# Kernel optimization log

Measured on AMD Instinct MI355X. Metric: run time of the kernel, lower is better.

The kernel has to match this reference:

```python
import jax, jax.numpy as jnp
import numpy as np

B, L, D, H, R, E = 4, 2048, 256, 4, 128, 32768
HD = D // H  # head dim of long-range attention
FF = 4 * D   # positionwise FFN hidden
NEG_SLOPE = 0.2  # GATConv leaky_relu slope


def setup_inputs() -> dict:
    key = jax.random.key(0)
    ks = jax.random.split(key, 16)
    n = lambda k, sh: jax.random.normal(k, sh, dtype=jnp.float32) * 0.05
    z = lambda sh: jnp.zeros(sh, dtype=jnp.float32)
    o = lambda sh: jnp.ones(sh, dtype=jnp.float32)
    return {
        "s": jax.random.normal(ks[0], (B, L, D), dtype=jnp.float32),
        "gat_W": n(ks[1], (D, H * D)),
        "gat_att_src": n(ks[2], (H, D)),
        "gat_att_dst": n(ks[3], (H, D)),
        "gat_b": z((H * D,)),
        "short_W": n(ks[4], (H * D, D)), "short_b": z((D,)),
        "q_W": n(ks[5], (D, D)), "q_b": z((D,)),
        "k_W": n(ks[6], (D, D)), "k_b": z((D,)),
        "v_W": n(ks[7], (D, D)), "v_b": z((D,)),
        "o_W": n(ks[8], (D, D)), "o_b": z((D,)),
        "p_W": n(ks[9], (D, R)), "p_b": z((R,)),
        "lnq_g": o((D,)), "lnq_b": z((D,)),
        "lnk_g": o((D,)), "lnk_b": z((D,)),
        "lnv_g": o((D,)), "lnv_b": z((D,)),
        "ln1_g": o((D,)), "ln1_b": z((D,)),
        "ln2_g": o((D,)), "ln2_b": z((D,)),
        "f1_W": n(ks[10], (D, FF)), "f1_b": z((FF,)),
        "f2_W": n(ks[11], (FF, D)), "f2_b": z((D,)),
        "edge_index": jax.random.randint(ks[12], (2, E), 0, L, dtype=jnp.int32),
    }


def _ln(x, g, b, eps=1e-5):
    mu = jnp.mean(x, -1, keepdims=True)
    var = jnp.mean(jnp.square(x - mu), -1, keepdims=True)
    return (x - mu) * jax.lax.rsqrt(var + eps) * g + b


def _forward(p, edge_index):
    s = p["s"]
    loop = jnp.arange(L, dtype=edge_index.dtype)  # add_self_loops=True
    src = jnp.concatenate([edge_index[0], loop])
    dst = jnp.concatenate([edge_index[1], loop])

    def gat_one(x):  # x: [L, D] -> [L, H*D]  (PyG GATConv, concat=True)
        h = (x @ p["gat_W"]).reshape(L, H, D)
        a_src = jnp.einsum("nhc,hc->nh", h, p["gat_att_src"])
        a_dst = jnp.einsum("nhc,hc->nh", h, p["gat_att_dst"])
        e = jax.nn.leaky_relu(a_src[src] + a_dst[dst], NEG_SLOPE)  # [Etot, H]
        m = jax.ops.segment_max(e, dst, num_segments=L)            # scatter softmax
        ex = jnp.exp(e - m[dst])
        den = jax.ops.segment_sum(ex, dst, num_segments=L)
        alpha = ex / den[dst]
        out = jax.ops.segment_sum(h[src] * alpha[:, :, None], dst, num_segments=L)
        return out.reshape(L, H * D) + p["gat_b"]

    short = jax.vmap(gat_one)(s) @ p["short_W"] + p["short_b"]  # [B,L,D]

    # DynamicLongRange (Linformer-style dynamic projection)
    q = _ln(s @ p["q_W"] + p["q_b"], p["lnq_g"], p["lnq_b"])
    k = _ln(s @ p["k_W"] + p["k_b"], p["lnk_g"], p["lnk_b"])
    v = _ln(s @ p["v_W"] + p["v_b"], p["lnv_g"], p["lnv_b"])
    pm = jax.nn.softmax(k @ p["p_W"] + p["p_b"], axis=1)          # [B,L,R], softmax over seq
    k_c = jnp.einsum("blr,bld->brd", pm, k).reshape(B, R, H, HD)
    v_c = jnp.einsum("blr,bld->brd", pm, v).reshape(B, R, H, HD)
    q_h = q.reshape(B, L, H, HD)
    scores = jnp.einsum("blhd,brhd->bhlr", q_h, k_c) / jnp.sqrt(jnp.float32(HD))
    probs = jax.nn.softmax(scores, axis=-1)
    lng = jnp.einsum("bhlr,brhd->blhd", probs, v_c).reshape(B, L, D)
    lng = lng @ p["o_W"] + p["o_b"]

    # fuse short + long, residual + LN, then positionwise FFN + residual + LN
    h1 = _ln(s + short + lng, p["ln1_g"], p["ln1_b"])
    ff = jax.nn.relu(h1 @ p["f1_W"] + p["f1_b"]) @ p["f2_W"] + p["f2_b"]
    return _ln(h1 + ff, p["ln2_g"], p["ln2_b"])


def reference(s, gat_W, gat_att_src, gat_att_dst, gat_b, short_W, short_b,
              q_W, q_b, k_W, k_b, v_W, v_b, o_W, o_b, p_W, p_b,
              lnq_g, lnq_b, lnk_g, lnk_b, lnv_g, lnv_b,
              ln1_g, ln1_b, ln2_g, ln2_b, f1_W, f1_b, f2_W, f2_b, edge_index):
    p = dict(s=s, gat_W=gat_W, gat_att_src=gat_att_src, gat_att_dst=gat_att_dst,
             gat_b=gat_b, short_W=short_W, short_b=short_b, q_W=q_W, q_b=q_b,
             k_W=k_W, k_b=k_b, v_W=v_W, v_b=v_b, o_W=o_W, o_b=o_b, p_W=p_W,
             p_b=p_b, lnq_g=lnq_g, lnq_b=lnq_b, lnk_g=lnk_g, lnk_b=lnk_b,
             lnv_g=lnv_g, lnv_b=lnv_b, ln1_g=ln1_g, ln1_b=ln1_b, ln2_g=ln2_g,
             ln2_b=ln2_b, f1_W=f1_W, f1_b=f1_b, f2_W=f2_W, f2_b=f2_b)
    return _forward(p, edge_index)
```

## Files before the change

kernel.cpp:

```cpp
#include <hip/hip_runtime.h>
#include <math.h>

#define BB   4
#define LSEQ 2048
#define DV   256
#define HH   4
#define RR   128
#define EE   32768
#define ETOT (EE + LSEQ)
#define FFD  1024

typedef unsigned short u16;
typedef __attribute__((ext_vector_type(8))) short bf16x8;
typedef __attribute__((ext_vector_type(4))) float f32x4;

__device__ __forceinline__ u16 f2bf(float f) {
    union { float f; unsigned u; } x; x.f = f;
    unsigned r = x.u + 0x7fff + ((x.u >> 16) & 1);
    return (u16)(r >> 16);
}
__device__ __forceinline__ float bf2f(u16 u) {
    union { unsigned u; float f; } x; x.u = ((unsigned)u) << 16;
    return x.f;
}

__device__ __forceinline__ void gload16(const void* g, void* l) {
    __builtin_amdgcn_global_load_lds(
        (const __attribute__((address_space(1))) unsigned int*)g,
        (__attribute__((address_space(3))) unsigned int*)l, 16, 0, 0);
}

template<int BM, int BN, int OUTBF16, int ACT>
__global__ __launch_bounds__(256) void mfma_gemm_k(
    const u16* __restrict__ A, const u16* __restrict__ BT,
    const float* __restrict__ bias, void* __restrict__ Cv,
    int M, int N, int K, int lda, int ldb, int ldc,
    long bsA1, long bsA2, long bsB1, long bsB2, long bsC1, long bsC2,
    int subH, long pairB, long pairC, int ksl, int split, float alpha)
{
    constexpr int BK = 64;
    __shared__ u16 As[BM * BK];
    __shared__ u16 Bs[BN * BK];

    int z = blockIdx.z;
    int zb = z / subH, zh = z - zb * subH;
    int mtiles = M / BM;
    int pair = blockIdx.y / mtiles;
    int mt   = blockIdx.y - pair * mtiles;

    const u16* Ab = A  + zb * bsA1 + zh * bsA2;
    const u16* Bb = BT + zb * bsB1 + zh * bsB2 + (long)pair * pairB;
    int kstart = split ? zh * ksl : 0;
    int kcount = split ? ksl : K;
    int m0 = mt * BM, n0 = blockIdx.x * BN;

    int tid  = threadIdx.x;
    int wave = tid >> 6, lane = tid & 63;
    constexpr int WGN = (BN == 128) ? 2 : 1;
    constexpr int WGM = 4 / WGN;
    constexpr int MI  = BM / (WGM * 16);
    constexpr int NI  = BN / (WGN * 16);
    int wm = wave / WGN, wn = wave - wm * WGN;
    int wmo = wm * (MI * 16);
    int wno = wn * (NI * 16);

    f32x4 acc[MI][NI];
#pragma unroll
    for (int mi = 0; mi < MI; ++mi)
#pragma unroll
        for (int ni = 0; ni < NI; ++ni)
            acc[mi][ni] = (f32x4){0.f, 0.f, 0.f, 0.f};

    constexpr int AIT = (BM * BK / 8) / 256;
    constexpr int BIT = (BN * BK / 8) / 256;

    for (int k0 = 0; k0 < kcount; k0 += BK) {
        int kb = kstart + k0;
#pragma unroll
        for (int i = 0; i < AIT; ++i) {
            int p   = i * 256 + tid;
            int row = p >> 3;
            int kc  = (p & 7) ^ (row & 7);
            const u16* gp = Ab + (long)(m0 + row) * lda + kb + kc * 8;
            gload16(gp, (char*)As + (size_t)(i * 256 + wave * 64) * 16);
        }
#pragma unroll
        for (int i = 0; i < BIT; ++i) {
            int p   = i * 256 + tid;
            int row = p >> 3;
            int kc  = (p & 7) ^ (row & 7);
            const u16* gp = Bb + (long)(n0 + row) * ldb + kb + kc * 8;
            gload16(gp, (char*)Bs + (size_t)(i * 256 + wave * 64) * 16);
        }
        asm volatile("s_waitcnt vmcnt(0)");
        __syncthreads();

        const char* Ac = (const char*)As;
        const char* Bc = (const char*)Bs;
#pragma unroll
        for (int kh = 0; kh < 2; ++kh) {
            bf16x8 af[MI], bfr[NI];
            int kby = kh * 64 + ((lane >> 4) << 4);
#pragma unroll
            for (int mi = 0; mi < MI; ++mi) {
                int r = wmo + mi * 16 + (lane & 15);
                af[mi] = *(const bf16x8*)(Ac + r * 128 + (kby ^ ((r & 7) << 4)));
            }
#pragma unroll
            for (int ni = 0; ni < NI; ++ni) {
                int r = wno + ni * 16 + (lane & 15);
                bfr[ni] = *(const bf16x8*)(Bc + r * 128 + (kby ^ ((r & 7) << 4)));
            }
#pragma unroll
            for (int mi = 0; mi < MI; ++mi)
#pragma unroll
                for (int ni = 0; ni < NI; ++ni)
                    acc[mi][ni] = __builtin_amdgcn_mfma_f32_16x16x32_bf16(
                        af[mi], bfr[ni], acc[mi][ni], 0, 0, 0);
        }
        __syncthreads();
    }

    long cb = zb * bsC1 + zh * bsC2 + (long)pair * pairC;
#pragma unroll
    for (int mi = 0; mi < MI; ++mi) {
#pragma unroll
        for (int ni = 0; ni < NI; ++ni) {
            int col = n0 + wno + ni * 16 + (lane & 15);
            float bv = bias ? bias[col] : 0.f;
#pragma unroll
            for (int j = 0; j < 4; ++j) {
                int row = m0 + wmo + mi * 16 + ((lane >> 4) << 2) + j;
                float v = acc[mi][ni][j] * alpha + bv;
                if (ACT) v = fmaxf(v, 0.f);
                long idx = (long)row * ldc + col + cb;
                if (OUTBF16) ((u16*)Cv)[idx] = f2bf(v);
                else         ((float*)Cv)[idx] = v;
            }
        }
    }
}

__global__ __launch_bounds__(256) void attn_k(
    const u16* __restrict__ qb, const u16* __restrict__ kcb,
    const u16* __restrict__ vcT, u16* __restrict__ lngb)
{
    __shared__ u16 Ps[64 * 128];

    int bh = blockIdx.y;
    int b = bh >> 2, h = bh & 3;
    int l0 = blockIdx.x * 64;
    int tid = threadIdx.x, wave = tid >> 6, lane = tid & 63;
    int c = lane & 15, g = lane >> 4;

    const u16* kc = kcb + (long)b * (RR * DV) + h * 64;
    const u16* qg = qb + ((long)(b * LSEQ + l0)) * DV + h * 64;
    const u16* vg = vcT + ((long)b * DV + h * 64) * RR;

    f32x4 acc[8];
#pragma unroll
    for (int mi = 0; mi < 8; ++mi) acc[mi] = (f32x4){0.f, 0.f, 0.f, 0.f};

#pragma unroll
    for (int kh = 0; kh < 2; ++kh) {
        bf16x8 bq = *(const bf16x8*)(qg + (long)(wave * 16 + c) * DV + kh * 32 + g * 8);
#pragma unroll
        for (int mi = 0; mi < 8; ++mi) {
            bf16x8 af = *(const bf16x8*)(kc + (long)(mi * 16 + c) * DV + kh * 32 + g * 8);
            acc[mi] = __builtin_amdgcn_mfma_f32_16x16x32_bf16(af, bq, acc[mi], 0, 0, 0);
        }
    }

    float mx = -INFINITY;
#pragma unroll
    for (int mi = 0; mi < 8; ++mi)
#pragma unroll
        for (int j = 0; j < 4; ++j) {
            acc[mi][j] *= 0.125f;
            mx = fmaxf(mx, acc[mi][j]);
        }
    mx = fmaxf(mx, __shfl_xor(mx, 16));
    mx = fmaxf(mx, __shfl_xor(mx, 32));
    float den = 0.f;
#pragma unroll
    for (int mi = 0; mi < 8; ++mi)
#pragma unroll
        for (int j = 0; j < 4; ++j) {
            acc[mi][j] = __expf(acc[mi][j] - mx);
            den += acc[mi][j];
        }
    den += __shfl_xor(den, 16);
    den += __shfl_xor(den, 32);
    float inv = 1.0f / den;

    int l = wave * 16 + c;
#pragma unroll
    for (int mi = 0; mi < 8; ++mi) {
        short4 sv;
        sv.x = (short)f2bf(acc[mi][0] * inv);
        sv.y = (short)f2bf(acc[mi][1] * inv);
        sv.z = (short)f2bf(acc[mi][2] * inv);
        sv.w = (short)f2bf(acc[mi][3] * inv);
        int byte = l * 256 + ((mi * 32 + g * 8) ^ ((l & 7) << 4));
        *(short4*)((char*)Ps + byte) = sv;
    }
    __syncthreads();

    f32x4 a2[4];
#pragma unroll
    for (int ni = 0; ni < 4; ++ni) a2[ni] = (f32x4){0.f, 0.f, 0.f, 0.f};
#pragma unroll
    for (int kb = 0; kb < 4; ++kb) {
        int kby = kb * 64 + (g << 4);
        bf16x8 pa = *(const bf16x8*)((char*)Ps + l * 256 + (kby ^ ((l & 7) << 4)));
#pragma unroll
        for (int ni = 0; ni < 4; ++ni) {
            bf16x8 vf = *(const bf16x8*)(vg + (long)(ni * 16 + c) * RR + kb * 32 + g * 8);
            a2[ni] = __builtin_amdgcn_mfma_f32_16x16x32_bf16(pa, vf, a2[ni], 0, 0, 0);
        }
    }
#pragma unroll
    for (int ni = 0; ni < 4; ++ni)
#pragma unroll
        for (int j = 0; j < 4; ++j) {
            int lr = wave * 16 + g * 4 + j;
            int dh = ni * 16 + c;
            lngb[((long)(b * LSEQ + l0 + lr)) * DV + h * 64 + dh] = f2bf(a2[ni][j]);
        }
}

struct WTD { const float* src; u16* dst; int K, N, toff; };
struct WTA { WTD d[9]; };

__global__ __launch_bounds__(256) void wtrans_all_k(WTA a)
{
    int bid = blockIdx.x;
    int di = 0;
#pragma unroll
    for (int i = 1; i < 9; ++i) if (bid >= a.d[i].toff) di = i;
    const float* src = a.d[di].src;
    u16* dst = a.d[di].dst;
    int K = a.d[di].K, N = a.d[di].N;
    int tix = bid - a.d[di].toff;
    int nx = N >> 5;
    int tn = tix % nx, tk = tix / nx;
    int n0 = tn * 32, k0 = tk * 32;

    __shared__ float t[32][33];
    int tx = threadIdx.x & 31, ty = threadIdx.x >> 5;
#pragma unroll
    for (int i = 0; i < 32; i += 8)
        t[ty + i][tx] = src[(long)(k0 + ty + i) * N + n0 + tx];
    __syncthreads();
#pragma unroll
    for (int i = 0; i < 32; i += 8)
        dst[(long)(n0 + ty + i) * K + k0 + tx] = f2bf(t[tx][ty + i]);
}

__global__ __launch_bounds__(256) void ttrans_k(const u16* __restrict__ in,
                                                u16* __restrict__ out,
                                                int R, int C, long isb, long osb)
{
    in  += blockIdx.z * isb;
    out += blockIdx.z * osb;
    __shared__ u16 t[32][33];
    int c0 = blockIdx.x * 32, r0 = blockIdx.y * 32;
    int tx = threadIdx.x & 31, ty = threadIdx.x >> 5;
#pragma unroll
    for (int i = 0; i < 32; i += 8)
        t[ty + i][tx] = in[(long)(r0 + ty + i) * C + c0 + tx];
    __syncthreads();
#pragma unroll
    for (int i = 0; i < 32; i += 8)
        out[(long)(c0 + ty + i) * R + r0 + tx] = t[tx][ty + i];
}

__global__ void castcat_k(const float* __restrict__ in, u16* __restrict__ out,
                          const float* qb_, const float* kb_, const float* vb_,
                          float* qkvb, int* icnt)
{
    int bid = blockIdx.x;
    if (bid < 2048) {
        int i = (bid * 256 + threadIdx.x) * 4;
        float4 v = *(const float4*)(in + i);
        out[i]     = f2bf(v.x);
        out[i + 1] = f2bf(v.y);
        out[i + 2] = f2bf(v.z);
        out[i + 3] = f2bf(v.w);
    } else if (bid == 2048) {
        int i = threadIdx.x;
#pragma unroll
        for (int rep = 0; rep < 3; ++rep) {
            int j = i + rep * 256;
            qkvb[j] = (j < 256) ? qb_[j] : ((j < 512) ? kb_[j - 256] : vb_[j - 512]);
        }
    } else {
        int t = (bid - 2049) * 256 + threadIdx.x;
        if (t < 512) ((int4*)icnt)[t] = (int4){0, 0, 0, 0};
    }
}

__global__ __launch_bounds__(256) void gat_att_k(
    const u16* __restrict__ h, const float* __restrict__ att_src,
    const float* __restrict__ att_dst, float* __restrict__ a_src,
    float* __restrict__ a_dst)
{
    int row  = blockIdx.x * 4 + (threadIdx.x >> 6);
    int lane = threadIdx.x & 63;
    int c0   = lane * 16;
    int head = lane >> 4;

    float as[16], ad[16];
#pragma unroll
    for (int i = 0; i < 16; ++i) { as[i] = att_src[c0 + i]; ad[i] = att_dst[c0 + i]; }

    const u16* hr = h + (long)row * (HH * DV) + c0;
    bf16x8 v0 = *(const bf16x8*)(hr);
    bf16x8 v1 = *(const bf16x8*)(hr + 8);
    float ps = 0.f, pd = 0.f;
#pragma unroll
    for (int i = 0; i < 8; ++i) {
        float f0 = bf2f((u16)v0[i]), f1 = bf2f((u16)v1[i]);
        ps += f0 * as[i] + f1 * as[i + 8];
        pd += f0 * ad[i] + f1 * ad[i + 8];
    }
#pragma unroll
    for (int m = 1; m <= 8; m <<= 1) {
        ps += __shfl_xor(ps, m);
        pd += __shfl_xor(pd, m);
    }
    if ((lane & 15) == 0) {
        a_src[(long)row * HH + head] = ps;
        a_dst[(long)row * HH + head] = pd;
    }
}

__global__ void csr_count_k(const int* __restrict__ ei, int* __restrict__ cnt)
{
    int i = blockIdx.x * blockDim.x + threadIdx.x;
    if (i >= ETOT) return;
    int dst = (i < EE) ? ei[EE + i] : (i - EE);
    atomicAdd(&cnt[dst], 1);
}

__global__ __launch_bounds__(256) void csr_scan_k(const int* __restrict__ cnt, int* __restrict__ off)
{
    __shared__ int chunk[256];
    int tid = threadIdx.x;
    int base = tid * 8;
    int loc[8];
    int s = 0;
#pragma unroll
    for (int i = 0; i < 8; ++i) { loc[i] = s; s += cnt[base + i]; }
    chunk[tid] = s;
    __syncthreads();
    for (int st = 1; st < 256; st <<= 1) {
        int v = (tid >= st) ? chunk[tid - st] : 0;
        __syncthreads();
        chunk[tid] += v;
        __syncthreads();
    }
    int pre = (tid == 0) ? 0 : chunk[tid - 1];
#pragma unroll
    for (int i = 0; i < 8; ++i) off[base + i] = pre + loc[i];
    if (tid == 255) off[LSEQ] = chunk[255];
}

__global__ void csr_fill_k(const int* __restrict__ ei, const int* __restrict__ off,
                           int* __restrict__ cnt, int* __restrict__ bucket)
{
    int i = blockIdx.x * blockDim.x + threadIdx.x;
    if (i >= ETOT) return;
    int dst = (i < EE) ? ei[EE + i] : (i - EE);
    int p = atomicSub(&cnt[dst], 1) - 1;
    bucket[off[dst] + p] = i;
}

__global__ __launch_bounds__(256) void gat_gather_k(
    const u16* __restrict__ h, const int* __restrict__ ei,
    const int* __restrict__ off, const int* __restrict__ bucket,
    const float* __restrict__ a_src, const float* __restrict__ a_dst,
    const float* __restrict__ gat_b, u16* __restrict__ out)
{
    int wv = threadIdx.x >> 6, lane = threadIdx.x & 63;
    int n = blockIdx.x * 4 + wv;
    int b = blockIdx.y;
    int beg = off[n], deg = off[n + 1] - beg;

    __shared__ int   src_sh[4][64];
    __shared__ float ex_sh[4][64][4];

    const float* asrc_b = a_src + (long)b * LSEQ * HH;
    const float4 ad4 = *(const float4*)(a_dst + ((long)b * LSEQ + n) * HH);
    float adst[4] = { ad4.x, ad4.y, ad4.z, ad4.w };

    int hd = lane >> 4;
    const u16* hb = h + (long)b * LSEQ * (HH * DV) + lane * 16;
    float acc[16];
#pragma unroll
    for (int i = 0; i < 16; ++i) acc[i] = 0.f;
    float sm[4] = { 0.f, 0.f, 0.f, 0.f };

    for (int c0 = 0; c0 < deg; c0 += 64) {
        int idx = c0 + lane;
        if (idx < deg) {
            int eid = bucket[beg + idx];
            int src = (eid < EE) ? ei[eid] : (eid - EE);
            src_sh[wv][lane] = src;
            float4 as4 = *(const float4*)(asrc_b + (long)src * HH);
            float as[4] = { as4.x, as4.y, as4.z, as4.w };
#pragma unroll
            for (int hh = 0; hh < 4; ++hh) {
                float e = as[hh] + adst[hh];
                e = (e >= 0.f) ? e : 0.2f * e;
                float ex = __expf(e);
                ex_sh[wv][lane][hh] = ex;
                sm[hh] += ex;
            }
        }
        int cn = deg - c0; if (cn > 64) cn = 64;
#pragma unroll 2
        for (int j = 0; j < cn; ++j) {
            int src = src_sh[wv][j];
            float al = ex_sh[wv][j][hd];
            const u16* p = hb + (long)src * (HH * DV);
            bf16x8 v0 = *(const bf16x8*)p;
            bf16x8 v1 = *(const bf16x8*)(p + 8);
#pragma unroll
            for (int i = 0; i < 8; ++i) {
                acc[i]     += al * bf2f((u16)v0[i]);
                acc[i + 8] += al * bf2f((u16)v1[i]);
            }
        }
    }

#pragma unroll
    for (int hh = 0; hh < 4; ++hh)
#pragma unroll
        for (int m = 32; m >= 1; m >>= 1)
            sm[hh] += __shfl_xor(sm[hh], m);
    float inv = 1.0f / sm[hd];

    u16 o16[16];
    const float* gb = gat_b + lane * 16;
#pragma unroll
    for (int i = 0; i < 16; ++i) o16[i] = f2bf(acc[i] * inv + gb[i]);
    uint4* op = (uint4*)(out + ((long)b * LSEQ + n) * (HH * DV) + lane * 16);
    op[0] = ((uint4*)o16)[0];
    op[1] = ((uint4*)o16)[1];
}

__global__ __launch_bounds__(256) void ln_cast3_k(
    const u16* __restrict__ x,
    const float* g0, const float* b0, const float* g1, const float* b1,
    const float* g2, const float* b2,
    u16* o0, u16* o1, u16* o2)
{
    int seg = blockIdx.y;
    long row = blockIdx.x;
    int tid = threadIdx.x;
    const float* g = (seg == 0) ? g0 : (seg == 1) ? g1 : g2;
    const float* bt = (seg == 0) ? b0 : (seg == 1) ? b1 : b2;
    u16* o = (seg == 0) ? o0 : (seg == 1) ? o1 : o2;

    float v = bf2f(x[row * 768 + seg * 256 + tid]);
    __shared__ float red[256];
    red[tid] = v; __syncthreads();
    for (int s = 128; s > 0; s >>= 1) { if (tid < s) red[tid] += red[tid + s]; __syncthreads(); }
    float mu = red[0] * (1.0f / DV);
    __syncthreads();
    float d = v - mu;
    red[tid] = d * d; __syncthreads();
    for (int s = 128; s > 0; s >>= 1) { if (tid < s) red[tid] += red[tid + s]; __syncthreads(); }
    float r = rsqrtf(red[0] * (1.0f / DV) + 1e-5f);
    o[row * DV + tid] = f2bf(d * r * g[tid] + bt[tid]);
}

__global__ __launch_bounds__(256) void ln_mix_k(
    const float* __restrict__ x0, const u16* __restrict__ x1,
    const u16* __restrict__ x2, const float* __restrict__ g,
    const float* __restrict__ bta, u16* __restrict__ outb)
{
    long row = blockIdx.x;
    int tid = threadIdx.x;
    long base = row * DV + tid;
    float v = x0[base] + bf2f(x1[base]) + bf2f(x2[base]);
    __shared__ float red[256];
    red[tid] = v; __syncthreads();
    for (int s = 128; s > 0; s >>= 1) { if (tid < s) red[tid] += red[tid + s]; __syncthreads(); }
    float mu = red[0] * (1.0f / DV);
    __syncthreads();
    float d = v - mu;
    red[tid] = d * d; __syncthreads();
    for (int s = 128; s > 0; s >>= 1) { if (tid < s) red[tid] += red[tid + s]; __syncthreads(); }
    float r = rsqrtf(red[0] * (1.0f / DV) + 1e-5f);
    outb[base] = f2bf(d * r * g[tid] + bta[tid]);
}

__global__ __launch_bounds__(256) void ln_bb_k(
    const u16* __restrict__ x0, const u16* __restrict__ x1,
    const float* __restrict__ g, const float* __restrict__ bta,
    float* __restrict__ out)
{
    long row = blockIdx.x;
    int tid = threadIdx.x;
    long base = row * DV + tid;
    float v = bf2f(x0[base]) + bf2f(x1[base]);
    __shared__ float red[256];
    red[tid] = v; __syncthreads();
    for (int s = 128; s > 0; s >>= 1) { if (tid < s) red[tid] += red[tid + s]; __syncthreads(); }
    float mu = red[0] * (1.0f / DV);
    __syncthreads();
    float d = v - mu;
    red[tid] = d * d; __syncthreads();
    for (int s = 128; s > 0; s >>= 1) { if (tid < s) red[tid] += red[tid + s]; __syncthreads(); }
    float r = rsqrtf(red[0] * (1.0f / DV) + 1e-5f);
    out[base] = d * r * g[tid] + bta[tid];
}

__global__ __launch_bounds__(256) void colsoftmax_k(const float* __restrict__ pm,
                                                    u16* __restrict__ pmT)
{
    int r = blockIdx.x;
    int b = blockIdx.y;
    int tid = threadIdx.x, wave = tid >> 6, lane = tid & 63;
    const float* base = pm + (long)b * LSEQ * RR + r;
    u16* obase = pmT + ((long)b * RR + r) * LSEQ;

    float x[8];
#pragma unroll
    for (int i = 0; i < 8; ++i) x[i] = base[(long)(tid + i * 256) * RR];

    __shared__ float red[4];
    __shared__ float m_sh, d_sh;
    float mx = x[0];
#pragma unroll
    for (int i = 1; i < 8; ++i) mx = fmaxf(mx, x[i]);
#pragma unroll
    for (int m = 32; m >= 1; m >>= 1) mx = fmaxf(mx, __shfl_xor(mx, m));
    if (lane == 0) red[wave] = mx;
    __syncthreads();
    if (tid == 0) m_sh = fmaxf(fmaxf(red[0], red[1]), fmaxf(red[2], red[3]));
    __syncthreads();
    float m = m_sh;
    float sm = 0.f;
#pragma unroll
    for (int i = 0; i < 8; ++i) { x[i] = __expf(x[i] - m); sm += x[i]; }
#pragma unroll
    for (int mm = 32; mm >= 1; mm >>= 1) sm += __shfl_xor(sm, mm);
    if (lane == 0) red[wave] = sm;
    __syncthreads();
    if (tid == 0) d_sh = red[0] + red[1] + red[2] + red[3];
    __syncthreads();
    float inv = 1.0f / d_sh;
#pragma unroll
    for (int i = 0; i < 8; ++i) obase[tid + i * 256] = f2bf(x[i] * inv);
}

__global__ __launch_bounds__(256) void reduce_kvc_k(
    const float* __restrict__ part, u16* __restrict__ kvcb, u16* __restrict__ vcT)
{
    int pb = blockIdx.z;
    int pair = pb >> 2, b = pb & 3;
    int r0 = blockIdx.y * 32, d0 = blockIdx.x * 64;
    int tid = threadIdx.x;
    __shared__ float t[32][65];
    const float* pp = part + (long)pb * (16 * 32768);
    int r = tid >> 6;
    int d = tid & 63;
#pragma unroll
    for (int i = 0; i < 8; ++i) {
        int rr = r0 + r + i * 4;
        float s = 0.f;
#pragma unroll
        for (int sp = 0; sp < 16; ++sp)
            s += pp[(long)sp * 32768 + rr * 256 + d0 + d];
        kvcb[(long)pb * 32768 + rr * 256 + d0 + d] = f2bf(s);
        t[r + i * 4][d] = s;
    }
    if (pair == 0) return;
    __syncthreads();
    int dd = tid >> 2, rb = (tid & 3) * 8;
    u16 o8[8];
#pragma unroll
    for (int k = 0; k < 8; ++k) o8[k] = f2bf(t[rb + k][dd]);
    *(uint4*)(vcT + ((long)(b * 256 + d0 + dd)) * 128 + r0 + rb) = *(uint4*)o8;
}

extern "C" void kernel_launch(void* const* d_in, const int* in_sizes, int n_in,
                              void* d_out, int out_size, void* d_ws, size_t ws_size,
                              hipStream_t stream)
{
    const float* s        = (const float*)d_in[0];
    const float* gat_W    = (const float*)d_in[1];
    const float* att_src  = (const float*)d_in[2];
    const float* att_dst  = (const float*)d_in[3];
    const float* gat_b    = (const float*)d_in[4];
    const float* short_W  = (const float*)d_in[5];
    const float* short_b  = (const float*)d_in[6];
    const float* q_W      = (const float*)d_in[7];
    const float* q_b      = (const float*)d_in[8];
    const float* k_W      = (const float*)d_in[9];
    const float* k_b      = (const float*)d_in[10];
    const float* v_W      = (const float*)d_in[11];
    const float* v_b      = (const float*)d_in[12];
    const float* o_W      = (const float*)d_in[13];
    const float* o_b      = (const float*)d_in[14];
    const float* p_W      = (const float*)d_in[15];
    const float* p_b      = (const float*)d_in[16];
    const float* lnq_g    = (const float*)d_in[17];
    const float* lnq_b    = (const float*)d_in[18];
    const float* lnk_g    = (const float*)d_in[19];
    const float* lnk_b    = (const float*)d_in[20];
    const float* lnv_g    = (const float*)d_in[21];
    const float* lnv_b    = (const float*)d_in[22];
    const float* ln1_g    = (const float*)d_in[23];
    const float* ln1_b    = (const float*)d_in[24];
    const float* ln2_g    = (const float*)d_in[25];
    const float* ln2_b    = (const float*)d_in[26];
    const float* f1_W     = (const float*)d_in[27];
    const float* f1_b     = (const float*)d_in[28];
    const float* f2_W     = (const float*)d_in[29];
    const float* f2_b     = (const float*)d_in[30];
    const int*   ei       = (const int*)d_in[31];
    float* out = (float*)d_out;

    const size_t MB = 1024 * 1024;
    char* W = (char*)d_ws;
    u16*   sb      = (u16*)(W);
    u16*   gatT    = (u16*)(W + 4*MB);
    u16*   shortT  = (u16*)(W + 4*MB + 524288);
    u16*   qkvT    = (u16*)(W + 4*MB + 1048576);
    u16*   oT      = (u16*)(W + 4*MB + 1441792);
    u16*   pT      = (u16*)(W + 4*MB + 1572864);
    u16*   f1T     = (u16*)(W + 4*MB + 1638400);
    u16*   f2T     = (u16*)(W + 4*MB + 2162688);
    float* qkvb    = (float*)(W + 4*MB + 2686976);
    int*   ioff    = (int*)(W + 4*MB + 2690048);
    int*   icnt    = (int*)(W + 4*MB + 2699264);
    int*   ibucket = (int*)(W + 4*MB + 2707456);
    u16*   h       = (u16*)(W + 8*MB);
    u16*   ffh     = (u16*)(W + 8*MB);
    u16*   gat_out = (u16*)(W + 24*MB);
    u16*   h1b     = (u16*)(W + 40*MB);
    u16*   shortb16= (u16*)(W + 44*MB);
    u16*   qkvb16  = (u16*)(W + 48*MB);
    float* pmraw   = (float*)(W + 48*MB);
    float* part    = (float*)(W + 48*MB);
    u16*   lngb    = (u16*)(W + 48*MB);
    u16*   lng2b   = (u16*)(W + 64*MB);
    u16*   qb      = (u16*)(W + 72*MB);
    u16*   kvb     = (u16*)(W + 76*MB);
    u16*   ff2b    = (u16*)(W + 76*MB);
    u16*   kvT     = (u16*)(W + 84*MB);
    u16*   pmT     = (u16*)(W + 92*MB);
    u16*   kvcb    = (u16*)(W + 94*MB);
    u16*   vcT     = (u16*)(W + 94*MB + 524288);
    float* a_src   = (float*)(W + 95*MB);
    float* a_dst   = (float*)(W + 95*MB + 131072);

    const int ML = BB * LSEQ;

    WTA wa;
    wa.d[0] = { gat_W,   gatT,            256, 1024, 0    };
    wa.d[1] = { short_W, shortT,         1024,  256, 256  };
    wa.d[2] = { q_W,     qkvT,            256,  256, 512  };
    wa.d[3] = { k_W,     qkvT + 65536,    256,  256, 576  };
    wa.d[4] = { v_W,     qkvT + 131072,   256,  256, 640  };
    wa.d[5] = { o_W,     oT,              256,  256, 704  };
    wa.d[6] = { p_W,     pT,              256,  128, 768  };
    wa.d[7] = { f1_W,    f1T,             256, 1024, 800  };
    wa.d[8] = { f2_W,    f2T,            1024,  256, 1056 };
    wtrans_all_k<<<1312, 256, 0, stream>>>(wa);
    castcat_k<<<2051, 256, 0, stream>>>(s, sb, q_b, k_b, v_b, qkvb, icnt);

    csr_count_k<<<(ETOT + 255) / 256, 256, 0, stream>>>(ei, icnt);
    csr_scan_k<<<1, 256, 0, stream>>>(icnt, ioff);
    csr_fill_k<<<(ETOT + 255) / 256, 256, 0, stream>>>(ei, ioff, icnt, ibucket);

    mfma_gemm_k<128, 128, 1, 0><<<dim3(8, 64, 1), 256, 0, stream>>>(
        sb, gatT, nullptr, h, ML, 1024, 256, 256, 256, 1024,
        0, 0, 0, 0, 0, 0, 1, 0, 0, 0, 0, 1.f);
    gat_att_k<<<ML / 4, 256, 0, stream>>>(h, att_src, att_dst, a_src, a_dst);
    gat_gather_k<<<dim3(LSEQ / 4, BB), 256, 0, stream>>>(h, ei, ioff, ibucket,
                                                         a_src, a_dst, gat_b, gat_out);
    mfma_gemm_k<64, 128, 1, 0><<<dim3(2, 128, 1), 256, 0, stream>>>(
        gat_out, shortT, short_b, shortb16, ML, 256, 1024, 1024, 1024, 256,
        0, 0, 0, 0, 0, 0, 1, 0, 0, 0, 0, 1.f);

    mfma_gemm_k<64, 128, 1, 0><<<dim3(6, 128, 1), 256, 0, stream>>>(
        sb, qkvT, qkvb, qkvb16, ML, 768, 256, 256, 256, 768,
        0, 0, 0, 0, 0, 0, 1, 0, 0, 0, 0, 1.f);
    ln_cast3_k<<<dim3(ML, 3), 256, 0, stream>>>(qkvb16, lnq_g, lnq_b, lnk_g, lnk_b,
                                                lnv_g, lnv_b, qb, kvb, kvb + 2097152);

    mfma_gemm_k<64, 64, 0, 0><<<dim3(2, 128, 1), 256, 0, stream>>>(
        kvb, pT, p_b, pmraw, ML, 128, 256, 256, 256, 128,
        0, 0, 0, 0, 0, 0, 1, 0, 0, 0, 0, 1.f);
    colsoftmax_k<<<dim3(RR, BB), 256, 0, stream>>>(pmraw, pmT);

    ttrans_k<<<dim3(8, 64, 8), 256, 0, stream>>>(kvb, kvT, 2048, 256, 524288, 524288);

    mfma_gemm_k<128, 128, 0, 0><<<dim3(2, 2, 64), 256, 0, stream>>>(
        pmT, kvT, nullptr, part, 128, 256, 2048, 2048, 2048, 256,
        262144, 0, 524288, 0, 524288, 32768, 16, 2097152, 2097152, 128, 1, 1.f);
    reduce_kvc_k<<<dim3(4, 4, 8), 256, 0, stream>>>(part, kvcb, vcT);

    attn_k<<<dim3(LSEQ / 64, BB * HH), 256, 0, stream>>>(qb, kvcb, vcT, lngb);

    mfma_gemm_k<64, 128, 1, 0><<<dim3(2, 128, 1), 256, 0, stream>>>(
        lngb, oT, o_b, lng2b, ML, 256, 256, 256, 256, 256,
        0, 0, 0, 0, 0, 0, 1, 0, 0, 0, 0, 1.f);

    ln_mix_k<<<ML, 256, 0, stream>>>(s, shortb16, lng2b, ln1_g, ln1_b, h1b);

    mfma_gemm_k<128, 128, 1, 1><<<dim3(8, 64, 1), 256, 0, stream>>>(
        h1b, f1T, f1_b, ffh, ML, 1024, 256, 256, 256, 1024,
        0, 0, 0, 0, 0, 0, 1, 0, 0, 0, 0, 1.f);
    mfma_gemm_k<64, 128, 1, 0><<<dim3(2, 128, 1), 256, 0, stream>>>(
        ffh, f2T, f2_b, ff2b, ML, 256, 1024, 1024, 1024, 256,
        0, 0, 0, 0, 0, 0, 1, 0, 0, 0, 0, 1.f);

    ln_bb_k<<<ML, 256, 0, stream>>>(h1b, ff2b, ln2_g, ln2_b, out);
}
```

Measured before the change: 239.4 us.

## Fuse layernorm epilogues into full-row GEMMs and drop separate transpose kernel

```diff
diff --git a/kernel.cpp b/kernel.cpp
--- a/kernel.cpp
+++ b/kernel.cpp
@@ -141,6 +141,189 @@
     }
 }
 
+template<int MODE>
+__global__ __launch_bounds__(256) void gemm_ln_k(
+    const u16* __restrict__ A, const u16* __restrict__ BT,
+    const float* __restrict__ bias, int K, int lda,
+    const float* __restrict__ lg0, const float* __restrict__ lb0,
+    const float* __restrict__ lg1, const float* __restrict__ lb1,
+    const float* __restrict__ lg2, const float* __restrict__ lb2,
+    const float* __restrict__ resF, const u16* __restrict__ resB,
+    u16* __restrict__ outRM, u16* __restrict__ outRM2,
+    u16* __restrict__ outT, float* __restrict__ outF)
+{
+    constexpr int BK = 64;
+    __shared__ char smem[40960];
+    __shared__ float redS[64][4], redQ[64][4];
+    u16* Asm = (u16*)smem;
+    u16* Bsm = (u16*)(smem + 8192);
+
+    int seg = blockIdx.x;
+    int m0 = blockIdx.y * 64;
+    int n0 = seg * 256;
+    int tid = threadIdx.x, wave = tid >> 6, lane = tid & 63;
+    int c = lane & 15, g = lane >> 4;
+
+    f32x4 acc[4][4];
+#pragma unroll
+    for (int mi = 0; mi < 4; ++mi)
+#pragma unroll
+        for (int ni = 0; ni < 4; ++ni)
+            acc[mi][ni] = (f32x4){0.f, 0.f, 0.f, 0.f};
+
+    for (int k0 = 0; k0 < K; k0 += BK) {
+#pragma unroll
+        for (int i = 0; i < 2; ++i) {
+            int p   = i * 256 + tid;
+            int row = p >> 3;
+            int kc  = (p & 7) ^ (row & 7);
+            gload16(A + (long)(m0 + row) * lda + k0 + kc * 8,
+                    smem + (size_t)(i * 256 + wave * 64) * 16);
+        }
+#pragma unroll
+        for (int i = 0; i < 8; ++i) {
+            int p   = i * 256 + tid;
+            int row = p >> 3;
+            int kc  = (p & 7) ^ (row & 7);
+            gload16(BT + (long)(n0 + row) * K + k0 + kc * 8,
+                    smem + 8192 + (size_t)(i * 256 + wave * 64) * 16);
+        }
+        asm volatile("s_waitcnt vmcnt(0)");
+        __syncthreads();
+
+        const char* Ac = (const char*)Asm;
+        const char* Bc = (const char*)Bsm;
+#pragma unroll
+        for (int kh = 0; kh < 2; ++kh) {
+            bf16x8 af[4], bfr[4];
+            int kby = kh * 64 + (g << 4);
+#pragma unroll
+            for (int mi = 0; mi < 4; ++mi) {
+                int r = mi * 16 + c;
+                af[mi] = *(const bf16x8*)(Ac + r * 128 + (kby ^ ((r & 7) << 4)));
+            }
+#pragma unroll
+            for (int ni = 0; ni < 4; ++ni) {
+                int r = wave * 64 + ni * 16 + c;
+                bfr[ni] = *(const bf16x8*)(Bc + r * 128 + (kby ^ ((r & 7) << 4)));
+            }
+#pragma unroll
+            for (int mi = 0; mi < 4; ++mi)
+#pragma unroll
+                for (int ni = 0; ni < 4; ++ni)
+                    acc[mi][ni] = __builtin_amdgcn_mfma_f32_16x16x32_bf16(
+                        af[mi], bfr[ni], acc[mi][ni], 0, 0, 0);
+        }
+        __syncthreads();
+    }
+
+#pragma unroll
+    for (int mi = 0; mi < 4; ++mi)
+#pragma unroll
+        for (int ni = 0; ni < 4; ++ni) {
+            int colL = wave * 64 + ni * 16 + c;
+            float bv = bias[n0 + colL];
+#pragma unroll
+            for (int j = 0; j < 4; ++j) {
+                int row = mi * 16 + g * 4 + j;
+                float v = acc[mi][ni][j] + bv;
+                if (MODE == 1) {
+                    long idx = (long)(m0 + row) * 256 + colL;
+                    v += resF[idx] + bf2f(resB[idx]);
+                }
+                if (MODE == 2) {
+                    long idx = (long)(m0 + row) * 256 + colL;
+                    v += bf2f(resB[idx]);
+                }
+                acc[mi][ni][j] = v;
+            }
+        }
+
+#pragma unroll
+    for (int mi = 0; mi < 4; ++mi)
+#pragma unroll
+        for (int j = 0; j < 4; ++j) {
+            float s1 = 0.f, q1 = 0.f;
+#pragma unroll
+            for (int ni = 0; ni < 4; ++ni) {
+                float v = acc[mi][ni][j];
+                s1 += v; q1 += v * v;
+            }
+#pragma unroll
+            for (int m = 1; m <= 8; m <<= 1) {
+                s1 += __shfl_xor(s1, m);
+                q1 += __shfl_xor(q1, m);
+            }
+            if (c == 0) {
+                int row = mi * 16 + g * 4 + j;
+                redS[row][wave] = s1;
+                redQ[row][wave] = q1;
+            }
+        }
+    __syncthreads();
+
+    const float* gam;
+    const float* bet;
+    if (MODE == 0) {
+        gam = (seg == 0) ? lg0 : (seg == 1) ? lg1 : lg2;
+        bet = (seg == 0) ? lb0 : (seg == 1) ? lb1 : lb2;
+    } else { gam = lg0; bet = lb0; }
+
+    u16* T = (u16*)smem;
+
+    float gv[4], bv2[4];
+#pragma unroll
+    for (int ni = 0; ni < 4; ++ni) {
+        int colL = wave * 64 + ni * 16 + c;
+        gv[ni] = gam[colL];
+        bv2[ni] = bet[colL];
+    }
+
+#pragma unroll
+    for (int mi = 0; mi < 4; ++mi)
+#pragma unroll
+        for (int j = 0; j < 4; ++j) {
+            int row = mi * 16 + g * 4 + j;
+            float S = redS[row][0] + redS[row][1] + redS[row][2] + redS[row][3];
+            float Q = redQ[row][0] + redQ[row][1] + redQ[row][2] + redQ[row][3];
+            float mu = S * (1.0f / 256.f);
+            float var = Q * (1.0f / 256.f) - mu * mu;
+            float rs = rsqrtf(var + 1e-5f);
+#pragma unroll
+            for (int ni = 0; ni < 4; ++ni) {
+                int colL = wave * 64 + ni * 16 + c;
+                float o = (acc[mi][ni][j] - mu) * rs * gv[ni] + bv2[ni];
+                long idx = (long)(m0 + row) * 256 + colL;
+                if (MODE == 0) {
+                    u16 ob = f2bf(o);
+                    if (seg == 0)      outRM[idx]  = ob;
+                    else if (seg == 1) { outRM2[idx] = ob; T[colL * 65 + row] = ob; }
+                    else               T[colL * 65 + row] = ob;
+                } else if (MODE == 1) {
+                    outRM[idx] = f2bf(o);
+                } else {
+                    outF[idx] = o;
+                }
+            }
+        }
+
+    if (MODE == 0 && seg >= 1) {
+        __syncthreads();
+        int b = m0 >> 11;
+        int l0 = m0 & 2047;
+        u16* dst = outT + ((seg == 2) ? 2097152 : 0)
+                 + (long)b * 524288 + (long)tid * 2048 + l0;
+        const u16* src = T + tid * 65;
+#pragma unroll
+        for (int i = 0; i < 8; ++i) {
+            u16 tmp[8];
+#pragma unroll
+            for (int k2 = 0; k2 < 8; ++k2) tmp[k2] = src[i * 8 + k2];
+            *(uint4*)(dst + i * 8) = *(uint4*)tmp;
+        }
+    }
+}
+
 __global__ __launch_bounds__(256) void attn_k(
     const u16* __restrict__ qb, const u16* __restrict__ kcb,
     const u16* __restrict__ vcT, u16* __restrict__ lngb)
@@ -255,24 +438,6 @@
 #pragma unroll
     for (int i = 0; i < 32; i += 8)
         dst[(long)(n0 + ty + i) * K + k0 + tx] = f2bf(t[tx][ty + i]);
-}
-
-__global__ __launch_bounds__(256) void ttrans_k(const u16* __restrict__ in,
-                                                u16* __restrict__ out,
-                                                int R, int C, long isb, long osb)
-{
-    in  += blockIdx.z * isb;
-    out += blockIdx.z * osb;
-    __shared__ u16 t[32][33];
-    int c0 = blockIdx.x * 32, r0 = blockIdx.y * 32;
-    int tx = threadIdx.x & 31, ty = threadIdx.x >> 5;
-#pragma unroll
-    for (int i = 0; i < 32; i += 8)
-        t[ty + i][tx] = in[(long)(r0 + ty + i) * C + c0 + tx];
-    __syncthreads();
-#pragma unroll
-    for (int i = 0; i < 32; i += 8)
-        out[(long)(c0 + ty + i) * R + r0 + tx] = t[tx][ty + i];
 }
 
 __global__ void castcat_k(const float* __restrict__ in, u16* __restrict__ out,
@@ -448,74 +613,6 @@
     uint4* op = (uint4*)(out + ((long)b * LSEQ + n) * (HH * DV) + lane * 16);
     op[0] = ((uint4*)o16)[0];
     op[1] = ((uint4*)o16)[1];
-}
-
-__global__ __launch_bounds__(256) void ln_cast3_k(
-    const u16* __restrict__ x,
-    const float* g0, const float* b0, const float* g1, const float* b1,
-    const float* g2, const float* b2,
-    u16* o0, u16* o1, u16* o2)
-{
-    int seg = blockIdx.y;
-    long row = blockIdx.x;
-    int tid = threadIdx.x;
-    const float* g = (seg == 0) ? g0 : (seg == 1) ? g1 : g2;
-    const float* bt = (seg == 0) ? b0 : (seg == 1) ? b1 : b2;
-    u16* o = (seg == 0) ? o0 : (seg == 1) ? o1 : o2;
-
-    float v = bf2f(x[row * 768 + seg * 256 + tid]);
-    __shared__ float red[256];
-    red[tid] = v; __syncthreads();
-    for (int s = 128; s > 0; s >>= 1) { if (tid < s) red[tid] += red[tid + s]; __syncthreads(); }
-    float mu = red[0] * (1.0f / DV);
-    __syncthreads();
-    float d = v - mu;
-    red[tid] = d * d; __syncthreads();
-    for (int s = 128; s > 0; s >>= 1) { if (tid < s) red[tid] += red[tid + s]; __syncthreads(); }
-    float r = rsqrtf(red[0] * (1.0f / DV) + 1e-5f);
-    o[row * DV + tid] = f2bf(d * r * g[tid] + bt[tid]);
-}
-
-__global__ __launch_bounds__(256) void ln_mix_k(
-    const float* __restrict__ x0, const u16* __restrict__ x1,
-    const u16* __restrict__ x2, const float* __restrict__ g,
-    const float* __restrict__ bta, u16* __restrict__ outb)
-{
-    long row = blockIdx.x;
-    int tid = threadIdx.x;
-    long base = row * DV + tid;
-    float v = x0[base] + bf2f(x1[base]) + bf2f(x2[base]);
-    __shared__ float red[256];
-    red[tid] = v; __syncthreads();
-    for (int s = 128; s > 0; s >>= 1) { if (tid < s) red[tid] += red[tid + s]; __syncthreads(); }
-    float mu = red[0] * (1.0f / DV);
-    __syncthreads();
-    float d = v - mu;
-    red[tid] = d * d; __syncthreads();
-    for (int s = 128; s > 0; s >>= 1) { if (tid < s) red[tid] += red[tid + s]; __syncthreads(); }
-    float r = rsqrtf(red[0] * (1.0f / DV) + 1e-5f);
-    outb[base] = f2bf(d * r * g[tid] + bta[tid]);
-}
-
-__global__ __launch_bounds__(256) void ln_bb_k(
-    const u16* __restrict__ x0, const u16* __restrict__ x1,
-    const float* __restrict__ g, const float* __restrict__ bta,
-    float* __restrict__ out)
-{
-    long row = blockIdx.x;
-    int tid = threadIdx.x;
-    long base = row * DV + tid;
-    float v = bf2f(x0[base]) + bf2f(x1[base]);
-    __shared__ float red[256];
-    red[tid] = v; __syncthreads();
-    for (int s = 128; s > 0; s >>= 1) { if (tid < s) red[tid] += red[tid + s]; __syncthreads(); }
-    float mu = red[0] * (1.0f / DV);
-    __syncthreads();
-    float d = v - mu;
-    red[tid] = d * d; __syncthreads();
-    for (int s = 128; s > 0; s >>= 1) { if (tid < s) red[tid] += red[tid + s]; __syncthreads(); }
-    float r = rsqrtf(red[0] * (1.0f / DV) + 1e-5f);
-    out[base] = d * r * g[tid] + bta[tid];
 }
 
 __global__ __launch_bounds__(256) void colsoftmax_k(const float* __restrict__ pm,
@@ -644,14 +741,11 @@
     u16*   gat_out = (u16*)(W + 24*MB);
     u16*   h1b     = (u16*)(W + 40*MB);
     u16*   shortb16= (u16*)(W + 44*MB);
-    u16*   qkvb16  = (u16*)(W + 48*MB);
     float* pmraw   = (float*)(W + 48*MB);
     float* part    = (float*)(W + 48*MB);
     u16*   lngb    = (u16*)(W + 48*MB);
-    u16*   lng2b   = (u16*)(W + 64*MB);
     u16*   qb      = (u16*)(W + 72*MB);
-    u16*   kvb     = (u16*)(W + 76*MB);
-    u16*   ff2b    = (u16*)(W + 76*MB);
+    u16*   kb      = (u16*)(W + 76*MB);
     u16*   kvT     = (u16*)(W + 84*MB);
     u16*   pmT     = (u16*)(W + 92*MB);
     u16*   kvcb    = (u16*)(W + 94*MB);
@@ -688,18 +782,15 @@
         gat_out, shortT, short_b, shortb16, ML, 256, 1024, 1024, 1024, 256,
         0, 0, 0, 0, 0, 0, 1, 0, 0, 0, 0, 1.f);
 
-    mfma_gemm_k<64, 128, 1, 0><<<dim3(6, 128, 1), 256, 0, stream>>>(
-        sb, qkvT, qkvb, qkvb16, ML, 768, 256, 256, 256, 768,
-        0, 0, 0, 0, 0, 0, 1, 0, 0, 0, 0, 1.f);
-    ln_cast3_k<<<dim3(ML, 3), 256, 0, stream>>>(qkvb16, lnq_g, lnq_b, lnk_g, lnk_b,
-                                                lnv_g, lnv_b, qb, kvb, kvb + 2097152);
+    gemm_ln_k<0><<<dim3(3, 128), 256, 0, stream>>>(
+        sb, qkvT, qkvb, 256, 256,
+        lnq_g, lnq_b, lnk_g, lnk_b, lnv_g, lnv_b,
+        nullptr, nullptr, qb, kb, kvT, nullptr);
 
     mfma_gemm_k<64, 64, 0, 0><<<dim3(2, 128, 1), 256, 0, stream>>>(
-        kvb, pT, p_b, pmraw, ML, 128, 256, 256, 256, 128,
+        kb, pT, p_b, pmraw, ML, 128, 256, 256, 256, 128,
         0, 0, 0, 0, 0, 0, 1, 0, 0, 0, 0, 1.f);
     colsoftmax_k<<<dim3(RR, BB), 256, 0, stream>>>(pmraw, pmT);
-
-    ttrans_k<<<dim3(8, 64, 8), 256, 0, stream>>>(kvb, kvT, 2048, 256, 524288, 524288);
 
     mfma_gemm_k<128, 128, 0, 0><<<dim3(2, 2, 64), 256, 0, stream>>>(
         pmT, kvT, nullptr, part, 128, 256, 2048, 2048, 2048, 256,
@@ -708,18 +799,17 @@
 
     attn_k<<<dim3(LSEQ / 64, BB * HH), 256, 0, stream>>>(qb, kvcb, vcT, lngb);
 
-    mfma_gemm_k<64, 128, 1, 0><<<dim3(2, 128, 1), 256, 0, stream>>>(
-        lngb, oT, o_b, lng2b, ML, 256, 256, 256, 256, 256,
-        0, 0, 0, 0, 0, 0, 1, 0, 0, 0, 0, 1.f);
-
-    ln_mix_k<<<ML, 256, 0, stream>>>(s, shortb16, lng2b, ln1_g, ln1_b, h1b);
+    gemm_ln_k<1><<<dim3(1, 128), 256, 0, stream>>>(
+        lngb, oT, o_b, 256, 256,
+        ln1_g, ln1_b, nullptr, nullptr, nullptr, nullptr,
+        s, shortb16, h1b, nullptr, nullptr, nullptr);
 
     mfma_gemm_k<128, 128, 1, 1><<<dim3(8, 64, 1), 256, 0, stream>>>(
         h1b, f1T, f1_b, ffh, ML, 1024, 256, 256, 256, 1024,
         0, 0, 0, 0, 0, 0, 1, 0, 0, 0, 0, 1.f);
-    mfma_gemm_k<64, 128, 1, 0><<<dim3(2, 128, 1), 256, 0, stream>>>(
-        ffh, f2T, f2_b, ff2b, ML, 256, 1024, 1024, 1024, 256,
-        0, 0, 0, 0, 0, 0, 1, 0, 0, 0, 0, 1.f);
-
-    ln_bb_k<<<ML, 256, 0, stream>>>(h1b, ff2b, ln2_g, ln2_b, out);
-}
+
+    gemm_ln_k<2><<<dim3(1, 128), 256, 0, stream>>>(
+        ffh, f2T, f2_b, 1024, 1024,
+        ln2_g, ln2_b, nullptr, nullptr, nullptr, nullptr,
+        nullptr, h1b, nullptr, nullptr, nullptr, out);
+}
```

Result: faster. 220.0 us (-8.1%).
